# Performance work log

Measured on AMD Instinct MI355X. Metric: run time of the kernel, lower is better.

Reference implementation:

```python
import jax, jax.numpy as jnp
import numpy as np

N_NODES = 30000
N_EDGES = 480000
IN_FEATS = 256
N_HEADS = 8
OUT_FEATS = 32
EDGE_FEATS = 64
NUM_ETYPES = 8
NEG_SLOPE = 0.2


def setup_inputs() -> dict:
    key = jax.random.key(0)
    ks = jax.random.split(key, 14)
    s = 0.05
    return {
        "feat": jax.random.normal(ks[0], (N_NODES, IN_FEATS), dtype=jnp.float32),
        "e_feat": jax.random.randint(ks[1], (N_EDGES,), 0, NUM_ETYPES, dtype=jnp.int32),
        "src": jax.random.randint(ks[2], (N_EDGES,), 0, N_NODES, dtype=jnp.int32),
        "dst": jax.random.randint(ks[3], (N_EDGES,), 0, N_NODES, dtype=jnp.int32),
        # learned params (torch nn.Linear stores weight as [out, in])
        "fc_W": jax.random.normal(ks[4], (N_HEADS * OUT_FEATS, IN_FEATS), dtype=jnp.float32) * s,
        "edge_emb": jax.random.normal(ks[5], (NUM_ETYPES, EDGE_FEATS), dtype=jnp.float32) * s,
        "w_r": jnp.ones((NUM_ETYPES, 1), dtype=jnp.float32),  # init constant 1.0
        "W1": jax.random.normal(ks[6], (EDGE_FEATS * 2, EDGE_FEATS), dtype=jnp.float32) * s,
        "b1": jnp.zeros((EDGE_FEATS * 2,), dtype=jnp.float32),
        "W2": jax.random.normal(ks[7], (EDGE_FEATS * N_HEADS, EDGE_FEATS * 2), dtype=jnp.float32) * s,
        "b2": jnp.zeros((EDGE_FEATS * N_HEADS,), dtype=jnp.float32),
        "attn_l": jax.random.normal(ks[8], (1, N_HEADS, OUT_FEATS), dtype=jnp.float32) * s,
        "attn_r": jax.random.normal(ks[9], (1, N_HEADS, OUT_FEATS), dtype=jnp.float32) * s,
        "attn_e": jax.random.normal(ks[10], (1, N_HEADS, EDGE_FEATS), dtype=jnp.float32) * s,
    }


def reference(feat, e_feat, src, dst, fc_W, edge_emb, w_r, W1, b1, W2, b2,
              attn_l, attn_r, attn_e):
    # node projection: [N, H, D]
    feat_src = (feat @ fc_W.T).reshape(N_NODES, N_HEADS, OUT_FEATS)

    # edge-type embedding -> MLP -> [E, H, edge_feats]
    e_emb = edge_emb[e_feat]                                  # [E, EF]
    h = jax.nn.relu(e_emb @ W1.T + b1)                        # [E, 2*EF]
    e_proc = (h @ W2.T + b2).reshape(-1, N_HEADS, EDGE_FEATS)  # [E, H, EF]

    ee = jnp.sum(e_proc * attn_e, axis=-1)                    # [E, H]
    el = jnp.sum(feat_src * attn_l, axis=-1)                  # [N, H]
    er = jnp.sum(feat_src * attn_r, axis=-1)                  # [N, H]

    logits = jax.nn.leaky_relu(el[src] + er[dst] + ee, NEG_SLOPE)
    logits = logits * w_r[e_feat]                             # relation weight, [E,1] bcast

    # edge_softmax: segment softmax over destination nodes
    emax = jax.ops.segment_max(logits, dst, num_segments=N_NODES)  # [N, H]
    ex = jnp.exp(logits - emax[dst])                               # [E, H]
    denom = jax.ops.segment_sum(ex, dst, num_segments=N_NODES)     # [N, H]
    a = ex / denom[dst]                                            # [E, H]

    # weighted scatter-sum aggregation: rst[v] = sum_{e: dst(e)=v} a_e * feat_src[src(e)]
    msg = feat_src[src] * a[..., None]                             # [E, H, D]
    rst = jax.ops.segment_sum(msg, dst, num_segments=N_NODES)      # [N, H, D]

    return rst, a[..., None]
```

## Files before the change

kernel.cpp:

```cpp
#include <hip/hip_runtime.h>
#include <math.h>

#define N_NODES 30000
#define N_EDGES 480000
#define IN_FEATS 256
#define N_HEADS 8
#define OUT_FEATS 32
#define EDGE_FEATS 64
#define NUM_ETYPES 8
#define NEG_SLOPE 0.2f
#define HD 256

typedef __bf16 bf16_t;
typedef bf16_t bf16x8 __attribute__((ext_vector_type(8)));
typedef float f32x4 __attribute__((ext_vector_type(4)));
typedef unsigned short ushort8_t __attribute__((ext_vector_type(8)));

__device__ __forceinline__ unsigned short f2bf(float f) {
    unsigned u = __float_as_uint(f);
    u += 0x7fffu + ((u >> 16) & 1u);
    return (unsigned short)(u >> 16);
}
__device__ __forceinline__ float bf2f(unsigned short s) {
    return __uint_as_float(((unsigned)s) << 16);
}

__device__ __forceinline__ void gload_lds16(const void* g, void* l) {
    __builtin_amdgcn_global_load_lds(
        (const __attribute__((address_space(1))) unsigned int*)g,
        (__attribute__((address_space(3))) unsigned int*)l, 16, 0, 0);
}

__global__ __launch_bounds__(1024) void ee_all(
    const float* __restrict__ edge_emb,
    const float* __restrict__ W1, const float* __restrict__ b1,
    const float* __restrict__ W2, const float* __restrict__ b2,
    const float* __restrict__ attn_e, float* __restrict__ ee_tab) {
    __shared__ float h1S[1024];
    __shared__ float MS[1024];
    const int t0 = threadIdx.x;
    {
        int t = t0 >> 7, r = t0 & 127;
        const float4* Wv = (const float4*)(W1 + (size_t)r * EDGE_FEATS);
        const float4* Ev = (const float4*)(edge_emb + (size_t)t * EDGE_FEATS);
        float s = b1[r];
        #pragma unroll
        for (int q = 0; q < 16; q++) {
            float4 w = Wv[q], e = Ev[q];
            s += w.x * e.x + w.y * e.y + w.z * e.z + w.w * e.w;
        }
        h1S[t0] = fmaxf(s, 0.f);
    }
    {
        int h = t0 >> 7, k = t0 & 127;
        float s = 0.f;
        #pragma unroll 8
        for (int f = 0; f < EDGE_FEATS; f++)
            s = fmaf(attn_e[h * EDGE_FEATS + f],
                     W2[(size_t)(h * EDGE_FEATS + f) * (2 * EDGE_FEATS) + k], s);
        MS[t0] = s;
    }
    __syncthreads();
    if (t0 < 64) {
        int t = t0 >> 3, h = t0 & 7;
        float s = 0.f;
        for (int f = 0; f < EDGE_FEATS; f++)
            s = fmaf(attn_e[h * EDGE_FEATS + f], b2[h * EDGE_FEATS + f], s);
        for (int k = 0; k < 2 * EDGE_FEATS; k++)
            s = fmaf(MS[h * 128 + k], h1S[t * 128 + k], s);
        ee_tab[t0] = s;
    }
}

__global__ void cvt_hist(const float* __restrict__ feat, const float* __restrict__ fcW,
                         const int* __restrict__ dst,
                         unsigned short* __restrict__ featb, unsigned short* __restrict__ fcWb,
                         int* __restrict__ counts) {
    const int n1 = N_NODES * IN_FEATS / 4;
    const int n2 = IN_FEATS * HD / 4;
    const int tid0 = blockIdx.x * blockDim.x + threadIdx.x;
    const int stride = gridDim.x * blockDim.x;
    for (int i = tid0; i < n1 + n2; i += stride) {
        float4 v = (i < n1) ? ((const float4*)feat)[i] : ((const float4*)fcW)[i - n1];
        ushort4 o;
        o.x = f2bf(v.x); o.y = f2bf(v.y); o.z = f2bf(v.z); o.w = f2bf(v.w);
        if (i < n1) ((ushort4*)featb)[i] = o;
        else        ((ushort4*)fcWb)[i - n1] = o;
    }
    for (int e = tid0; e < N_EDGES; e += stride)
        atomicAdd(&counts[dst[e]], 1);
}

#define GBM 128
#define GBN 64
#define GBK 64
__global__ __launch_bounds__(256) void gemm_bf16(const unsigned short* __restrict__ A,
                                                 const unsigned short* __restrict__ B,
                                                 const float* __restrict__ attn_l,
                                                 const float* __restrict__ attn_r,
                                                 unsigned short* __restrict__ Cb,
                                                 float* __restrict__ el,
                                                 float* __restrict__ er) {
    __shared__ __align__(16) unsigned char As[GBM * GBK * 2];
    __shared__ __align__(16) unsigned char Bs[GBN * GBK * 2];
    const int tid = threadIdx.x;
    const int lane = tid & 63;
    const int wid = tid >> 6;
    const int wr = wid >> 1, wc = wid & 1;
    const int row0 = blockIdx.x * GBM;
    const int col0 = blockIdx.y * GBN;

    f32x4 acc[4][2] = {};

    for (int k0 = 0; k0 < IN_FEATS; k0 += GBK) {
        __syncthreads();
        #pragma unroll
        for (int i = 0; i < 4; i++) {
            int loff = wid * 4096 + i * 1024;
            int row = (loff >> 7) + (lane >> 3);
            int c = lane & 7;
            int gr = row0 + row; if (gr > N_NODES - 1) gr = N_NODES - 1;
            int gc = k0 + ((c ^ (row & 7)) << 3);
            gload_lds16(A + (size_t)gr * IN_FEATS + gc, As + loff + lane * 16);
        }
        #pragma unroll
        for (int i = 0; i < 2; i++) {
            int loff = wid * 2048 + i * 1024;
            int row = (loff >> 7) + (lane >> 3);
            int c = lane & 7;
            int gc = k0 + ((c ^ (row & 7)) << 3);
            gload_lds16(B + (size_t)(col0 + row) * IN_FEATS + gc, Bs + loff + lane * 16);
        }
        asm volatile("s_waitcnt vmcnt(0)" ::: "memory");
        __syncthreads();
        #pragma unroll
        for (int kk = 0; kk < 2; kk++) {
            bf16x8 af[4], bfr[2];
            const int g = kk * 4 + (lane >> 4);
            #pragma unroll
            for (int fm = 0; fm < 4; fm++) {
                int row = wr * 64 + fm * 16 + (lane & 15);
                af[fm] = *(const bf16x8*)(As + row * 128 + ((g ^ (row & 7)) << 4));
            }
            #pragma unroll
            for (int fn = 0; fn < 2; fn++) {
                int row = wc * 32 + fn * 16 + (lane & 15);
                bfr[fn] = *(const bf16x8*)(Bs + row * 128 + ((g ^ (row & 7)) << 4));
            }
            #pragma unroll
            for (int fm = 0; fm < 4; fm++)
                #pragma unroll
                for (int fn = 0; fn < 2; fn++)
                    acc[fm][fn] = __builtin_amdgcn_mfma_f32_16x16x32_bf16(
                        af[fm], bfr[fn], acc[fm][fn], 0, 0, 0);
        }
    }
    #pragma unroll
    for (int fm = 0; fm < 4; fm++) {
        #pragma unroll
        for (int r = 0; r < 4; r++) {
            int row = row0 + wr * 64 + fm * 16 + (lane >> 4) * 4 + r;
            if (row < N_NODES) {
                #pragma unroll
                for (int fn = 0; fn < 2; fn++) {
                    int col = col0 + wc * 32 + fn * 16 + (lane & 15);
                    Cb[(size_t)row * HD + col] = f2bf(acc[fm][fn][r]);
                }
            }
        }
    }
    const int h = col0 / 32 + wc;
    const int d0 = lane & 15;
    const float al0 = attn_l[h * 32 + d0],  al1 = attn_l[h * 32 + d0 + 16];
    const float ar0 = attn_r[h * 32 + d0],  ar1 = attn_r[h * 32 + d0 + 16];
    #pragma unroll
    for (int fm = 0; fm < 4; fm++) {
        #pragma unroll
        for (int r = 0; r < 4; r++) {
            float sl = acc[fm][0][r] * al0 + acc[fm][1][r] * al1;
            float sr = acc[fm][0][r] * ar0 + acc[fm][1][r] * ar1;
            #pragma unroll
            for (int m = 1; m <= 8; m <<= 1) {
                sl += __shfl_xor(sl, m);
                sr += __shfl_xor(sr, m);
            }
            int row = row0 + wr * 64 + fm * 16 + (lane >> 4) * 4 + r;
            if (d0 == 0 && row < N_NODES) {
                el[row * 8 + h] = sl;
                er[row * 8 + h] = sr;
            }
        }
    }
}

__global__ __launch_bounds__(1024) void scan_kernel(const int* __restrict__ counts,
                                                    int* __restrict__ offsets,
                                                    int* __restrict__ cursor) {
    __shared__ int buf[30720];
    __shared__ int sums[1024];
    const int t = threadIdx.x;
    const int per = 30;
    for (int i = t; i < 30720; i += 1024)
        buf[i] = (i < N_NODES) ? counts[i] : 0;
    __syncthreads();
    int s = 0;
    #pragma unroll
    for (int i = 0; i < per; i++) s += buf[t * per + i];
    sums[t] = s;
    __syncthreads();
    for (int off = 1; off < 1024; off <<= 1) {
        int v = (t >= off) ? sums[t - off] : 0;
        __syncthreads();
        sums[t] += v;
        __syncthreads();
    }
    int run = sums[t] - s;
    #pragma unroll
    for (int i = 0; i < per; i++) {
        int c = buf[t * per + i];
        buf[t * per + i] = run;
        run += c;
    }
    __syncthreads();
    for (int i = t; i < N_NODES; i += 1024) {
        int v = buf[i];
        offsets[i] = v; cursor[i] = v;
    }
}

__global__ void scatter_kernel(const int* __restrict__ dst, int* __restrict__ cursor,
                               int* __restrict__ sorted_eid) {
    int e = blockIdx.x * blockDim.x + threadIdx.x;
    if (e >= N_EDGES) return;
    int pos = atomicAdd(&cursor[dst[e]], 1);
    sorted_eid[pos] = e;
}

__global__ __launch_bounds__(256) void node_fused(
    const int* __restrict__ offsets, const int* __restrict__ counts,
    const int* __restrict__ sorted, const int* __restrict__ src,
    const int* __restrict__ etype,
    const float* __restrict__ el, const float* __restrict__ er,
    const float* __restrict__ ee_tab, const float* __restrict__ w_r,
    const unsigned short* __restrict__ fsb,
    float* __restrict__ rst, float* __restrict__ aOut) {
    __shared__ float eeS[64];
    __shared__ float wrS[8];
    __shared__ float lgS[4][64][8];
    if (threadIdx.x < 64) eeS[threadIdx.x] = ee_tab[threadIdx.x];
    if (threadIdx.x < 8)  wrS[threadIdx.x] = w_r[threadIdx.x];
    __syncthreads();
    const int wv = threadIdx.x >> 6, lane = threadIdx.x & 63;
    const int e_l = lane >> 3, h = lane & 7;
    const int el2 = lane >> 5;
    const int q = lane & 31;
    const int hq = q >> 2;
    const int fs_off = hq * OUT_FEATS + (q & 3) * 8;
    const int nstride = (int)gridDim.x * 4;

    for (int node = blockIdx.x * 4 + wv; node < N_NODES; node += nstride) {
        const int beg = offsets[node], cnt = counts[node];
        const float er_v = er[node * 8 + h];
        const int nch = (cnt + 7) >> 3;

        float m = -1e30f;
        for (int ch = 0; ch < nch; ch++) {
            int idx = ch * 8 + e_l;
            float lg = -1e30f;
            if (idx < cnt) {
                int eid = sorted[beg + idx];
                int s = src[eid], t = etype[eid];
                float x = el[s * 8 + h] + er_v + eeS[t * 8 + h];
                x = (x > 0.f) ? x : NEG_SLOPE * x;
                lg = x * wrS[t];
            }
            if (idx < 64) lgS[wv][idx][h] = lg;
            m = fmaxf(m, lg);
        }
        m = fmaxf(m, __shfl_xor(m, 8));
        m = fmaxf(m, __shfl_xor(m, 16));
        m = fmaxf(m, __shfl_xor(m, 32));

        float sum = 0.f;
        for (int ch = 0; ch < nch; ch++) {
            int idx = ch * 8 + e_l;
            if (idx < cnt) {
                float lg;
                if (idx < 64) lg = lgS[wv][idx][h];
                else {
                    int eid = sorted[beg + idx];
                    int s = src[eid], t = etype[eid];
                    float x = el[s * 8 + h] + er_v + eeS[t * 8 + h];
                    x = (x > 0.f) ? x : NEG_SLOPE * x;
                    lg = x * wrS[t];
                }
                sum += __expf(lg - m);
            }
        }
        sum += __shfl_xor(sum, 8);
        sum += __shfl_xor(sum, 16);
        sum += __shfl_xor(sum, 32);
        const float inv = 1.f / sum;

        float acc[8] = {};
        for (int ch = 0; ch < nch; ch++) {
            int idx = ch * 8 + e_l;
            float a = 0.f; int s = 0;
            if (idx < cnt) {
                int eid = sorted[beg + idx];
                s = src[eid];
                float lg;
                if (idx < 64) lg = lgS[wv][idx][h];
                else {
                    int t = etype[eid];
                    float x = el[s * 8 + h] + er_v + eeS[t * 8 + h];
                    x = (x > 0.f) ? x : NEG_SLOPE * x;
                    lg = x * wrS[t];
                }
                a = __expf(lg - m) * inv;
                aOut[(size_t)eid * 8 + h] = a;
            }
            #pragma unroll
            for (int j = 0; j < 8; j += 2) {
                int jj = j + el2;
                int sj = __shfl(s, jj * 8);
                float av = __shfl(a, jj * 8 + hq);
                ushort8_t u = *(const ushort8_t*)(fsb + (size_t)sj * HD + fs_off);
                #pragma unroll
                for (int d = 0; d < 8; d++)
                    acc[d] = fmaf(av, bf2f(u[d]), acc[d]);
            }
        }
        #pragma unroll
        for (int d = 0; d < 8; d++) acc[d] += __shfl_xor(acc[d], 32);
        *(float4*)(rst + (size_t)node * HD + q * 8 + el2 * 4) =
            make_float4(acc[el2 * 4 + 0], acc[el2 * 4 + 1],
                        acc[el2 * 4 + 2], acc[el2 * 4 + 3]);
    }
}

extern "C" void kernel_launch(void* const* d_in, const int* in_sizes, int n_in,
                              void* d_out, int out_size, void* d_ws, size_t ws_size,
                              hipStream_t stream) {
    const float* feat     = (const float*)d_in[0];
    const int*   e_feat   = (const int*)  d_in[1];
    const int*   src      = (const int*)  d_in[2];
    const int*   dst      = (const int*)  d_in[3];
    const float* fc_W     = (const float*)d_in[4];
    const float* edge_emb = (const float*)d_in[5];
    const float* w_r      = (const float*)d_in[6];
    const float* W1       = (const float*)d_in[7];
    const float* b1       = (const float*)d_in[8];
    const float* W2       = (const float*)d_in[9];
    const float* b2       = (const float*)d_in[10];
    const float* attn_l   = (const float*)d_in[11];
    const float* attn_r   = (const float*)d_in[12];
    const float* attn_e   = (const float*)d_in[13];

    char* ws = (char*)d_ws;
    unsigned short* featb  = (unsigned short*)(ws + 0);
    unsigned short* fsb    = (unsigned short*)(ws + 15360000);
    float*          el     = (float*)(ws + 30720000);
    float*          er     = (float*)(ws + 31680000);
    unsigned short* fcWb   = (unsigned short*)(ws + 32640000);
    float*          ee_tab = (float*)(ws + 32771072);
    int*            counts = (int*)(ws + 32771328);
    int*            offs   = (int*)(ws + 32891328);
    int*            cursor = (int*)(ws + 33011328);
    int*            sorted = (int*)(ws + 33131328);

    float* rst  = (float*)d_out;
    float* aOut = rst + (size_t)N_NODES * HD;

    hipMemsetAsync(counts, 0, 120000, stream);
    ee_all<<<1, 1024, 0, stream>>>(edge_emb, W1, b1, W2, b2, attn_e, ee_tab);
    cvt_hist<<<2048, 256, 0, stream>>>(feat, fc_W, dst, featb, fcWb, counts);
    scan_kernel<<<1, 1024, 0, stream>>>(counts, offs, cursor);
    scatter_kernel<<<(N_EDGES + 255) / 256, 256, 0, stream>>>(dst, cursor, sorted);
    gemm_bf16<<<dim3((N_NODES + GBM - 1) / GBM, HD / GBN), 256, 0, stream>>>(
        featb, fcWb, attn_l, attn_r, fsb, el, er);
    node_fused<<<2048, 256, 0, stream>>>(
        offs, counts, sorted, src, e_feat, el, er, ee_tab, w_r, fsb, rst, aOut);
}
```

Before: 276.1 us.

## Pack src/etype into sorted edge records and restructure per-node aggregation

The scatter kernel now writes packed (src*8+etype, eid) pairs into the CSR-sorted array, so the node kernel avoids the indirect src/etype gathers through the edge id. The node kernel switches from a grid-stride loop to one wave per node, with the grid sized to the node count. Aggregation now walks edges serially through LDS-staged source ids and attention weights, and each lane accumulates four output features over the full 256-wide row instead of splitting edges across half-waves. This removes dependent index loads and shuffles, at the cost of a doubled sorted-array write, a serial per-edge inner loop with narrower 8-byte feature loads, and LDS round trips.

Measured after the change: 256.8 us. 7.0% less time.

```diff
diff --git a/kernel.cpp b/kernel.cpp
--- a/kernel.cpp
+++ b/kernel.cpp
@@ -14,7 +14,6 @@
 typedef __bf16 bf16_t;
 typedef bf16_t bf16x8 __attribute__((ext_vector_type(8)));
 typedef float f32x4 __attribute__((ext_vector_type(4)));
-typedef unsigned short ushort8_t __attribute__((ext_vector_type(8)));
 
 __device__ __forceinline__ unsigned short f2bf(float f) {
     unsigned u = __float_as_uint(f);
@@ -228,18 +227,18 @@
     }
 }
 
-__global__ void scatter_kernel(const int* __restrict__ dst, int* __restrict__ cursor,
-                               int* __restrict__ sorted_eid) {
+__global__ void scatter_kernel(const int* __restrict__ dst, const int* __restrict__ src,
+                               const int* __restrict__ etype, int* __restrict__ cursor,
+                               int2* __restrict__ sorted2) {
     int e = blockIdx.x * blockDim.x + threadIdx.x;
     if (e >= N_EDGES) return;
     int pos = atomicAdd(&cursor[dst[e]], 1);
-    sorted_eid[pos] = e;
+    sorted2[pos] = make_int2(src[e] * 8 + etype[e], e);
 }
 
 __global__ __launch_bounds__(256) void node_fused(
     const int* __restrict__ offsets, const int* __restrict__ counts,
-    const int* __restrict__ sorted, const int* __restrict__ src,
-    const int* __restrict__ etype,
+    const int2* __restrict__ sorted2,
     const float* __restrict__ el, const float* __restrict__ er,
     const float* __restrict__ ee_tab, const float* __restrict__ w_r,
     const unsigned short* __restrict__ fsb,
@@ -247,96 +246,90 @@
     __shared__ float eeS[64];
     __shared__ float wrS[8];
     __shared__ float lgS[4][64][8];
+    __shared__ int   sS[4][8];
     if (threadIdx.x < 64) eeS[threadIdx.x] = ee_tab[threadIdx.x];
     if (threadIdx.x < 8)  wrS[threadIdx.x] = w_r[threadIdx.x];
     __syncthreads();
     const int wv = threadIdx.x >> 6, lane = threadIdx.x & 63;
+    const int node = blockIdx.x * 4 + wv;
+    if (node >= N_NODES) return;
+    const int beg = offsets[node], cnt = counts[node];
     const int e_l = lane >> 3, h = lane & 7;
-    const int el2 = lane >> 5;
-    const int q = lane & 31;
-    const int hq = q >> 2;
-    const int fs_off = hq * OUT_FEATS + (q & 3) * 8;
-    const int nstride = (int)gridDim.x * 4;
-
-    for (int node = blockIdx.x * 4 + wv; node < N_NODES; node += nstride) {
-        const int beg = offsets[node], cnt = counts[node];
-        const float er_v = er[node * 8 + h];
-        const int nch = (cnt + 7) >> 3;
-
-        float m = -1e30f;
-        for (int ch = 0; ch < nch; ch++) {
-            int idx = ch * 8 + e_l;
-            float lg = -1e30f;
-            if (idx < cnt) {
-                int eid = sorted[beg + idx];
-                int s = src[eid], t = etype[eid];
+    const float er_v = er[node * 8 + h];
+    const int nch = (cnt + 7) >> 3;
+
+    float m = -1e30f;
+    for (int ch = 0; ch < nch; ch++) {
+        int idx = ch * 8 + e_l;
+        float lg = -1e30f;
+        if (idx < cnt) {
+            int2 p = sorted2[beg + idx];
+            int s = p.x >> 3, t = p.x & 7;
+            float x = el[s * 8 + h] + er_v + eeS[t * 8 + h];
+            x = (x > 0.f) ? x : NEG_SLOPE * x;
+            lg = x * wrS[t];
+        }
+        if (idx < 64) lgS[wv][idx][h] = lg;
+        m = fmaxf(m, lg);
+    }
+    m = fmaxf(m, __shfl_xor(m, 8));
+    m = fmaxf(m, __shfl_xor(m, 16));
+    m = fmaxf(m, __shfl_xor(m, 32));
+
+    float sum = 0.f;
+    for (int ch = 0; ch < nch; ch++) {
+        int idx = ch * 8 + e_l;
+        if (idx < cnt) {
+            float lg;
+            if (idx < 64) lg = lgS[wv][idx][h];
+            else {
+                int2 p = sorted2[beg + idx];
+                int s = p.x >> 3, t = p.x & 7;
                 float x = el[s * 8 + h] + er_v + eeS[t * 8 + h];
                 x = (x > 0.f) ? x : NEG_SLOPE * x;
                 lg = x * wrS[t];
             }
-            if (idx < 64) lgS[wv][idx][h] = lg;
-            m = fmaxf(m, lg);
-        }
-        m = fmaxf(m, __shfl_xor(m, 8));
-        m = fmaxf(m, __shfl_xor(m, 16));
-        m = fmaxf(m, __shfl_xor(m, 32));
-
-        float sum = 0.f;
-        for (int ch = 0; ch < nch; ch++) {
-            int idx = ch * 8 + e_l;
-            if (idx < cnt) {
-                float lg;
-                if (idx < 64) lg = lgS[wv][idx][h];
-                else {
-                    int eid = sorted[beg + idx];
-                    int s = src[eid], t = etype[eid];
-                    float x = el[s * 8 + h] + er_v + eeS[t * 8 + h];
-                    x = (x > 0.f) ? x : NEG_SLOPE * x;
-                    lg = x * wrS[t];
-                }
-                sum += __expf(lg - m);
-            }
-        }
-        sum += __shfl_xor(sum, 8);
-        sum += __shfl_xor(sum, 16);
-        sum += __shfl_xor(sum, 32);
-        const float inv = 1.f / sum;
-
-        float acc[8] = {};
-        for (int ch = 0; ch < nch; ch++) {
-            int idx = ch * 8 + e_l;
-            float a = 0.f; int s = 0;
-            if (idx < cnt) {
-                int eid = sorted[beg + idx];
-                s = src[eid];
-                float lg;
-                if (idx < 64) lg = lgS[wv][idx][h];
-                else {
-                    int t = etype[eid];
-                    float x = el[s * 8 + h] + er_v + eeS[t * 8 + h];
-                    x = (x > 0.f) ? x : NEG_SLOPE * x;
-                    lg = x * wrS[t];
-                }
-                a = __expf(lg - m) * inv;
-                aOut[(size_t)eid * 8 + h] = a;
-            }
-            #pragma unroll
-            for (int j = 0; j < 8; j += 2) {
-                int jj = j + el2;
-                int sj = __shfl(s, jj * 8);
-                float av = __shfl(a, jj * 8 + hq);
-                ushort8_t u = *(const ushort8_t*)(fsb + (size_t)sj * HD + fs_off);
-                #pragma unroll
-                for (int d = 0; d < 8; d++)
-                    acc[d] = fmaf(av, bf2f(u[d]), acc[d]);
-            }
-        }
-        #pragma unroll
-        for (int d = 0; d < 8; d++) acc[d] += __shfl_xor(acc[d], 32);
-        *(float4*)(rst + (size_t)node * HD + q * 8 + el2 * 4) =
-            make_float4(acc[el2 * 4 + 0], acc[el2 * 4 + 1],
-                        acc[el2 * 4 + 2], acc[el2 * 4 + 3]);
-    }
+            sum += __expf(lg - m);
+        }
+    }
+    sum += __shfl_xor(sum, 8);
+    sum += __shfl_xor(sum, 16);
+    sum += __shfl_xor(sum, 32);
+    const float inv = 1.f / sum;
+
+    float acc0 = 0.f, acc1 = 0.f, acc2 = 0.f, acc3 = 0.f;
+    const int hq = lane >> 3;
+    for (int ch = 0; ch < nch; ch++) {
+        int idx = ch * 8 + e_l;
+        float a = 0.f; int s = 0;
+        if (idx < cnt) {
+            int2 p = sorted2[beg + idx];
+            s = p.x >> 3;
+            float lg;
+            if (idx < 64) lg = lgS[wv][idx][h];
+            else {
+                int t = p.x & 7;
+                float x = el[s * 8 + h] + er_v + eeS[t * 8 + h];
+                x = (x > 0.f) ? x : NEG_SLOPE * x;
+                lg = x * wrS[t];
+            }
+            a = __expf(lg - m) * inv;
+            aOut[(size_t)p.y * 8 + h] = a;
+        }
+        lgS[wv][idx & 63][h] = a;
+        if (h == 0) sS[wv][e_l] = s;
+        int lim = cnt - ch * 8; if (lim > 8) lim = 8;
+        for (int j = 0; j < lim; j++) {
+            int sj = sS[wv][j];
+            float av = lgS[wv][(ch * 8 + j) & 63][hq];
+            ushort4 u = *(const ushort4*)(fsb + (size_t)sj * HD + lane * 4);
+            acc0 = fmaf(av, bf2f(u.x), acc0);
+            acc1 = fmaf(av, bf2f(u.y), acc1);
+            acc2 = fmaf(av, bf2f(u.z), acc2);
+            acc3 = fmaf(av, bf2f(u.w), acc3);
+        }
+    }
+    *(float4*)(rst + (size_t)node * HD + lane * 4) = make_float4(acc0, acc1, acc2, acc3);
 }
 
 extern "C" void kernel_launch(void* const* d_in, const int* in_sizes, int n_in,
@@ -367,7 +360,7 @@
     int*            counts = (int*)(ws + 32771328);
     int*            offs   = (int*)(ws + 32891328);
     int*            cursor = (int*)(ws + 33011328);
-    int*            sorted = (int*)(ws + 33131328);
+    int2*           sorted2= (int2*)(ws + 33131328);
 
     float* rst  = (float*)d_out;
     float* aOut = rst + (size_t)N_NODES * HD;
@@ -376,9 +369,9 @@
     ee_all<<<1, 1024, 0, stream>>>(edge_emb, W1, b1, W2, b2, attn_e, ee_tab);
     cvt_hist<<<2048, 256, 0, stream>>>(feat, fc_W, dst, featb, fcWb, counts);
     scan_kernel<<<1, 1024, 0, stream>>>(counts, offs, cursor);
-    scatter_kernel<<<(N_EDGES + 255) / 256, 256, 0, stream>>>(dst, cursor, sorted);
+    scatter_kernel<<<(N_EDGES + 255) / 256, 256, 0, stream>>>(dst, src, e_feat, cursor, sorted2);
     gemm_bf16<<<dim3((N_NODES + GBM - 1) / GBM, HD / GBN), 256, 0, stream>>>(
         featb, fcWb, attn_l, attn_r, fsb, el, er);
-    node_fused<<<2048, 256, 0, stream>>>(
-        offs, counts, sorted, src, e_feat, el, er, ee_tab, w_r, fsb, rst, aOut);
-}
+    node_fused<<<(N_NODES + 3) / 4, 256, 0, stream>>>(
+        offs, counts, sorted2, el, er, ee_tab, w_r, fsb, rst, aOut);
+}
```
